# Performance work log

Hardware: AMD Instinct MI355X
Metric: run time of the kernel (lower is better)

The kernel has to match this reference:

```python
import jax, jax.numpy as jnp
import numpy as np

HEAD_SIZE = 64


def setup_inputs() -> dict:
    key = jax.random.key(0)
    k1, k2, k3, k4 = jax.random.split(key, 4)
    B, T, C, H = 8, 2048, 1024, HEAD_SIZE
    return {
        "idx": jax.random.normal(k1, (B, T, C), dtype=jnp.float32),
        "Wk": jax.random.normal(k2, (C, H), dtype=jnp.float32) * (C ** -0.5),
        "Wq": jax.random.normal(k3, (C, H), dtype=jnp.float32) * (C ** -0.5),
        "Wv": jax.random.normal(k4, (C, H), dtype=jnp.float32) * (C ** -0.5),
    }


def reference(idx, Wk, Wq, Wv):
    # idx: [B, T, C]; Wk/Wq/Wv: [C, H]
    B, T, C = idx.shape
    H = Wk.shape[1]
    k = idx @ Wk  # [B, T, H]
    q = idx @ Wq  # [B, T, H]
    v = idx @ Wv  # [B, T, H]
    # Faithful to source: wei = k @ q^T (note: k first, as written in the torch code)
    wei = jnp.einsum("bth,bsh->bts", k, q) * (H ** -0.5)  # [B, T, T]
    causal = jnp.tril(jnp.ones((T, T), dtype=bool))
    wei = jnp.where(causal, wei, -jnp.inf)
    wei = jax.nn.softmax(wei, axis=-1)
    # Dropout(0.5) treated as eval-mode identity (deterministic reference)
    out = jnp.einsum("bts,bsh->bth", wei, v)  # [B, T, H]
    return out
```

## Files before the change

kernel.cpp:

```cpp
#include <hip/hip_runtime.h>

#define B_ 8
#define T_ 2048
#define C_ 1024
#define H_ 64
#define BT_ (B_ * T_)

typedef float f32x4 __attribute__((ext_vector_type(4)));
typedef unsigned short u16x4 __attribute__((ext_vector_type(4)));
typedef unsigned short u16x8 __attribute__((ext_vector_type(8)));
typedef __bf16 bf16x8 __attribute__((ext_vector_type(8)));

static __device__ __forceinline__ unsigned short f2bf(float f) {
    unsigned int u = __builtin_bit_cast(unsigned int, f);
    u = (u + 0x7FFFu + ((u >> 16) & 1u)) >> 16;
    return (unsigned short)u;
}

static __device__ __forceinline__ f32x4 mfma16(u16x8 a, u16x8 b, f32x4 c) {
    return __builtin_amdgcn_mfma_f32_16x16x32_bf16(
        __builtin_bit_cast(bf16x8, a), __builtin_bit_cast(bf16x8, b), c, 0, 0, 0);
}

static __device__ __forceinline__ void cvtpk4(float a0, float a1, float a2, float a3,
                                              unsigned& d0, unsigned& d1) {
    asm("v_cvt_pk_bf16_f32 %0, %1, %2" : "=v"(d0) : "v"(a0), "v"(a1));
    asm("v_cvt_pk_bf16_f32 %0, %1, %2" : "=v"(d1) : "v"(a2), "v"(a3));
}

static __device__ __forceinline__ int Pof(int j) {
    return 5 - (j >= 2 ? 1 : 0) - (j >= 6 ? 1 : 0);
}
static __device__ __forceinline__ int offsof(int j) {
    return (j < 2) ? 5 * j : (j < 6 ? 4 * j + 2 : 3 * j + 8);
}

__global__ __launch_bounds__(256) void wprep(const float* __restrict__ Wk,
                                             const float* __restrict__ Wq,
                                             const float* __restrict__ Wv,
                                             unsigned short* __restrict__ wt) {
    __shared__ float tile[64][65];
    const int arr = blockIdx.x >> 4, ct = blockIdx.x & 15;
    const float* W = (arr == 0) ? Wk : ((arr == 1) ? Wq : Wv);
    const int tid = threadIdx.x;
    {
        int c = tid >> 2, seg = (tid & 3) << 4;
        const float* src = W + (size_t)(ct * 64 + c) * 64 + seg;
#pragma unroll
        for (int j = 0; j < 16; j += 4) {
            f32x4 v4 = *(const f32x4*)(src + j);
            tile[c][seg + j + 0] = v4[0];
            tile[c][seg + j + 1] = v4[1];
            tile[c][seg + j + 2] = v4[2];
            tile[c][seg + j + 3] = v4[3];
        }
    }
    __syncthreads();
    {
        int h = tid >> 2, cs = (tid & 3) << 4;
        unsigned short* dst = wt + (size_t)(arr * 64 + h) * 1024 + ct * 64 + cs;
#pragma unroll
        for (int j = 0; j < 16; ++j) dst[j] = f2bf(tile[cs + j][h]);
    }
}

__global__ __launch_bounds__(512, 4) void proj_gemm(const float* __restrict__ idx,
                                                    const unsigned short* __restrict__ wt,
                                                    unsigned short* __restrict__ kw,
                                                    unsigned short* __restrict__ qw,
                                                    unsigned short* __restrict__ vtw) {
    __shared__ unsigned short As[2][32 * 64];
    __shared__ unsigned short Bs[2][192 * 64];
    const int tid = threadIdx.x;
    const int lane = tid & 63, w = tid >> 6;
    const int g = lane >> 4, l15 = lane & 15;
    const int m0 = blockIdx.x * 32;
    const int arow = tid >> 4, aseg = tid & 15;

    f32x4 acc[3] = {};
    f32x4 areg[2];
    u16x8 breg[2][3];

    auto sload = [&](int set, int k0) {
        areg[set] = *(const f32x4*)(idx + (size_t)(m0 + arow) * 1024 + k0 + aseg * 4);
#pragma unroll
        for (int i = 0; i < 3; ++i) {
            int slot = i * 512 + tid, n = slot >> 3, u = slot & 7;
            breg[set][i] = *(const u16x8*)(wt + (size_t)n * 1024 + k0 + u * 8);
        }
    };
    auto swrite = [&](int set, int buf) {
        unsigned d0, d1;
        cvtpk4(areg[set][0], areg[set][1], areg[set][2], areg[set][3], d0, d1);
        int au = aseg >> 1, ah = aseg & 1;
        uint2 pk; pk.x = d0; pk.y = d1;
        *(uint2*)&As[buf][arow * 64 + ((au ^ (arow & 7)) * 8) + ah * 4] = pk;
#pragma unroll
        for (int i = 0; i < 3; ++i) {
            int slot = i * 512 + tid, n = slot >> 3, u = slot & 7;
            *(u16x8*)&Bs[buf][n * 64 + ((u ^ (n & 7)) * 8)] = breg[set][i];
        }
    };

    sload(0, 0);
    sload(1, 64);
    swrite(0, 0);
    __syncthreads();

    for (int kt = 0; kt < 16; ++kt) {
        const int cur = kt & 1;
        if (kt < 14) sload(cur, (kt + 2) * 64);
#pragma unroll
        for (int ks = 0; ks < 2; ++ks) {
            u16x8 a = *(const u16x8*)&As[cur][((w & 1) * 16 + l15) * 64 +
                                              (((ks * 4 + g) ^ (l15 & 7)) * 8)];
#pragma unroll
            for (int nf = 0; nf < 3; ++nf) {
                int n = (w >> 1) * 48 + nf * 16 + l15;
                u16x8 b = *(const u16x8*)&Bs[cur][n * 64 + (((ks * 4 + g) ^ (n & 7)) * 8)];
                acc[nf] = mfma16(a, b, acc[nf]);
            }
        }
        if (kt < 15) swrite(cur ^ 1, cur ^ 1);
        __syncthreads();
    }

#pragma unroll
    for (int nf = 0; nf < 3; ++nf) {
        int nb = (w >> 1) * 3 + nf;
        int arr = nb >> 2;
        int nloc = ((nb & 3) << 4) + l15;
        f32x4 ac = acc[nf];
        int row = m0 + (w & 1) * 16 + g * 4;
        if (arr == 2) {
            u16x4 pk = {f2bf(ac[0]), f2bf(ac[1]), f2bf(ac[2]), f2bf(ac[3])};
            *(u16x4*)&vtw[(size_t)nloc * BT_ + row] = pk;
        } else {
            unsigned short* dst = arr ? qw : kw;
            dst[(size_t)(row + 0) * 64 + nloc] = f2bf(ac[0]);
            dst[(size_t)(row + 1) * 64 + nloc] = f2bf(ac[1]);
            dst[(size_t)(row + 2) * 64 + nloc] = f2bf(ac[2]);
            dst[(size_t)(row + 3) * 64 + nloc] = f2bf(ac[3]);
        }
    }
}

__global__ __launch_bounds__(512, 2) void attn_part(const unsigned short* __restrict__ kw,
                                                    const unsigned short* __restrict__ qw,
                                                    const unsigned short* __restrict__ vtw,
                                                    float* __restrict__ Opart,
                                                    float* __restrict__ lpart) {
    __shared__ unsigned short q_s[2][64 * 64];
    __shared__ unsigned short v_s[2][64 * 64];
    __shared__ unsigned short p_s[8 * 32 * 64];
    const int tid = threadIdx.x;
    const int w = tid >> 6, lane = tid & 63;
    const int g = lane >> 4, l15 = lane & 15;
    const int bid = blockIdx.x;
    const int b = bid & 7;
    const int rem = bid >> 3;
    const int j = (rem < 10) ? (rem / 5) : (rem < 26 ? (rem - 2) >> 2 : (rem - 8) / 3);
    const int P = Pof(j);
    const int part = rem - offsof(j);
    const size_t base = (size_t)b * T_;
    const int tA0 = 128 * j + 16 * w;
    const int tB0 = 128 * (15 - j) + 16 * w;
    const int nS = 2 * (16 - j);
    unsigned short* p_my = p_s + w * 2048;
    const float SCL = 0.125f * 1.44269504f;
    const float MOFF = 16.0f;
    const int sr = tid >> 3, su = tid & 7;

    u16x8 kf[2][2];
#pragma unroll
    for (int tf = 0; tf < 2; ++tf) {
        const unsigned short* kr = kw + (size_t)(base + (tf ? tB0 : tA0) + l15) * 64;
        kf[tf][0] = *(const u16x8*)(kr + g * 8);
        kf[tf][1] = *(const u16x8*)(kr + 32 + g * 8);
    }

    f32x4 o[4][2] = {};
    float l_lane[2] = {0.f, 0.f};

    u16x8 tq, tv;
    auto sload = [&](int st) {
        int s0 = st << 6;
        tq = *(const u16x8*)(qw + (size_t)(base + s0 + sr) * 64 + su * 8);
        tv = *(const u16x8*)(vtw + (size_t)sr * BT_ + base + s0 + su * 8);
    };
    auto swrite = [&](int buf) {
        *(u16x8*)&q_s[buf][sr * 64 + ((su ^ (sr & 7)) * 8)] = tq;
        *(u16x8*)&v_s[buf][sr * 64 + ((su ^ (sr & 7)) * 8)] = tv;
    };

    sload(part);
    swrite(0);
    __syncthreads();

    int i = 0;
    for (int st = part; st < nS; st += P, ++i) {
        const int s0 = st << 6;
        const int buf = i & 1;
        const bool more = (st + P < nS);
        if (more) sload(st + P);
        const bool dA = (s0 <= tA0 + 15);
        const bool dB = (s0 <= tB0 + 15);

        u16x8 a[2][4];
#pragma unroll
        for (int ks = 0; ks < 2; ++ks)
#pragma unroll
            for (int sf = 0; sf < 4; ++sf)
                a[ks][sf] = *(const u16x8*)&q_s[buf][(sf * 16 + l15) * 64 +
                                                     (((ks * 4 + g) ^ (l15 & 7)) * 8)];

        f32x4 s_[4][2] = {};
        __builtin_amdgcn_s_setprio(1);
        if (dB) {
#pragma unroll
            for (int ks = 0; ks < 2; ++ks)
#pragma unroll
                for (int sf = 0; sf < 4; ++sf)
                    s_[sf][1] = mfma16(a[ks][sf], kf[1][ks], s_[sf][1]);
        }
        if (dA) {
#pragma unroll
            for (int ks = 0; ks < 2; ++ks)
#pragma unroll
                for (int sf = 0; sf < 4; ++sf)
                    s_[sf][0] = mfma16(a[ks][sf], kf[0][ks], s_[sf][0]);
        }
        __builtin_amdgcn_s_setprio(0);

#pragma unroll
        for (int tf_ = 1; tf_ >= 0; --tf_) {
            if (tf_ ? !dB : !dA) continue;
            const int tbase_ = tf_ ? tB0 : tA0;
            float pv[4][4];
#pragma unroll
            for (int sf = 0; sf < 4; ++sf)
#pragma unroll
                for (int r = 0; r < 4; ++r)
                    pv[sf][r] = exp2f(fmaf(s_[sf][tf_][r], SCL, -MOFF));
            if (s0 + 63 > tbase_) {
                const int t_ = tbase_ + l15;
#pragma unroll
                for (int sf = 0; sf < 4; ++sf)
#pragma unroll
                    for (int r = 0; r < 4; ++r) {
                        int sg = s0 + sf * 16 + g * 4 + r;
                        if (sg > t_) pv[sf][r] = 0.f;
                    }
            }
            float lacc = 0.f;
#pragma unroll
            for (int sf = 0; sf < 4; ++sf)
                lacc += (pv[sf][0] + pv[sf][1]) + (pv[sf][2] + pv[sf][3]);
            l_lane[tf_] += lacc;
            const int trow = tf_ * 16 + l15;
#pragma unroll
            for (int sf = 0; sf < 4; ++sf) {
                unsigned r0, r1;
                cvtpk4(pv[sf][0], pv[sf][1], pv[sf][2], pv[sf][3], r0, r1);
                int u16i = (sf * 2 + (g >> 1)) ^ (l15 & 7);
                uint2 pk; pk.x = r0; pk.y = r1;
                *(uint2*)&p_my[trow * 64 + u16i * 8 + (g & 1) * 4] = pk;
            }
        }

        u16x8 vf[2][4];
#pragma unroll
        for (int ks = 0; ks < 2; ++ks)
#pragma unroll
            for (int mf = 0; mf < 4; ++mf)
                vf[ks][mf] = *(const u16x8*)&v_s[buf][(mf * 16 + l15) * 64 +
                                                      (((ks * 4 + g) ^ (l15 & 7)) * 8)];
        __builtin_amdgcn_s_setprio(1);
#pragma unroll
        for (int ks = 0; ks < 2; ++ks) {
            if (dB) {
                u16x8 bp1 = *(const u16x8*)&p_my[(16 + l15) * 64 +
                                                 (((ks * 4 + g) ^ (l15 & 7)) * 8)];
#pragma unroll
                for (int mf = 0; mf < 4; ++mf)
                    o[mf][1] = mfma16(vf[ks][mf], bp1, o[mf][1]);
            }
            if (dA) {
                u16x8 bp0 = *(const u16x8*)&p_my[l15 * 64 +
                                                 (((ks * 4 + g) ^ (l15 & 7)) * 8)];
#pragma unroll
                for (int mf = 0; mf < 4; ++mf)
                    o[mf][0] = mfma16(vf[ks][mf], bp0, o[mf][0]);
            }
        }
        __builtin_amdgcn_s_setprio(0);

        if (more) swrite(buf ^ 1);
        __syncthreads();
    }

#pragma unroll
    for (int tf = 0; tf < 2; ++tf) {
        float ls = l_lane[tf];
        ls += __shfl_xor(ls, 16);
        ls += __shfl_xor(ls, 32);
        int rl = tf * 128 + w * 16 + l15;
        if (g == 0) lpart[(size_t)bid * 256 + rl] = ls;
#pragma unroll
        for (int mf = 0; mf < 4; ++mf)
            *(f32x4*)&Opart[(size_t)bid * 16384 + (size_t)rl * 64 + mf * 16 + g * 4] = o[mf][tf];
    }
}

__global__ __launch_bounds__(256) void attn_comb(const float* __restrict__ Opart,
                                                 const float* __restrict__ lpart,
                                                 float* __restrict__ out) {
    int gt = blockIdx.x * 256 + threadIdx.x;
    int row = gt >> 4;
    int h0 = (gt & 15) << 2;
    int b = row >> 11, t = row & 2047;
    int ti = t >> 7, rit = t & 127;
    int j = (ti < 8) ? ti : (15 - ti);
    int tf = (ti < 8) ? 0 : 1;
    int rl = tf * 128 + rit;
    int P = Pof(j), offs = offsof(j);
    f32x4 acc = {};
    float L = 0.f;
    for (int p = 0; p < P; ++p) {
        int pb = b + 8 * (offs + p);
        acc += *(const f32x4*)&Opart[(size_t)pb * 16384 + (size_t)rl * 64 + h0];
        L += lpart[(size_t)pb * 256 + rl];
    }
    float inv = 1.f / L;
    *(f32x4*)&out[(size_t)row * 64 + h0] = acc * inv;
}

extern "C" void kernel_launch(void* const* d_in, const int* in_sizes, int n_in,
                              void* d_out, int out_size, void* d_ws, size_t ws_size,
                              hipStream_t stream) {
    const float* idx = (const float*)d_in[0];
    const float* Wk = (const float*)d_in[1];
    const float* Wq = (const float*)d_in[2];
    const float* Wv = (const float*)d_in[3];
    float* out = (float*)d_out;

    unsigned short* wt = (unsigned short*)d_ws;
    unsigned short* kw = wt + 192 * 1024;
    unsigned short* qw = kw + (size_t)BT_ * 64;
    unsigned short* vtw = qw + (size_t)BT_ * 64;
    float* Opart = (float*)((char*)d_ws + (8u << 20));
    float* lpart = Opart + (size_t)256 * 16384;

    wprep<<<48, 256, 0, stream>>>(Wk, Wq, Wv, wt);
    proj_gemm<<<512, 512, 0, stream>>>(idx, wt, kw, qw, vtw);
    attn_part<<<256, 512, 0, stream>>>(kw, qw, vtw, Opart, lpart);
    attn_comb<<<1024, 256, 0, stream>>>(Opart, lpart, out);
}
```

Measured before the change: 50.72 us.

## Enlarge projection GEMM M-tile to 128 rows per block to reuse weight tile

The projection GEMM block now computes 128 rows instead of 32, with each wave holding a 4x3 grid of MFMA accumulators. Each staged weight tile in shared memory is therefore reused across four times more rows, cutting redundant weight loads from global memory. The cost is only 128 blocks on a GPU with many CUs, which lowers parallelism, plus more registers and LDS per block. The occupancy hint drops from 4 to 2 to match.

```diff
diff --git a/kernel.cpp b/kernel.cpp
--- a/kernel.cpp
+++ b/kernel.cpp
@@ -64,25 +64,29 @@
     }
 }
 
-__global__ __launch_bounds__(512, 4) void proj_gemm(const float* __restrict__ idx,
+__global__ __launch_bounds__(512, 2) void proj_gemm(const float* __restrict__ idx,
                                                     const unsigned short* __restrict__ wt,
                                                     unsigned short* __restrict__ kw,
                                                     unsigned short* __restrict__ qw,
                                                     unsigned short* __restrict__ vtw) {
-    __shared__ unsigned short As[2][32 * 64];
+    __shared__ unsigned short As[2][128 * 64];
     __shared__ unsigned short Bs[2][192 * 64];
     const int tid = threadIdx.x;
     const int lane = tid & 63, w = tid >> 6;
     const int g = lane >> 4, l15 = lane & 15;
-    const int m0 = blockIdx.x * 32;
-    const int arow = tid >> 4, aseg = tid & 15;
-
-    f32x4 acc[3] = {};
-    f32x4 areg[2];
+    const int m0 = blockIdx.x * 128;
+    const int arow = tid >> 2, aseg = tid & 3;
+
+    f32x4 acc[4][3] = {};
+    f32x4 areg[2][4];
     u16x8 breg[2][3];
 
     auto sload = [&](int set, int k0) {
-        areg[set] = *(const f32x4*)(idx + (size_t)(m0 + arow) * 1024 + k0 + aseg * 4);
+        const f32x4* src = (const f32x4*)(idx + (size_t)(m0 + arow) * 1024 + k0 + aseg * 16);
+        areg[set][0] = src[0];
+        areg[set][1] = src[1];
+        areg[set][2] = src[2];
+        areg[set][3] = src[3];
 #pragma unroll
         for (int i = 0; i < 3; ++i) {
             int slot = i * 512 + tid, n = slot >> 3, u = slot & 7;
@@ -90,11 +94,14 @@
         }
     };
     auto swrite = [&](int set, int buf) {
-        unsigned d0, d1;
-        cvtpk4(areg[set][0], areg[set][1], areg[set][2], areg[set][3], d0, d1);
-        int au = aseg >> 1, ah = aseg & 1;
-        uint2 pk; pk.x = d0; pk.y = d1;
-        *(uint2*)&As[buf][arow * 64 + ((au ^ (arow & 7)) * 8) + ah * 4] = pk;
+        u16x8 c0, c1;
+#pragma unroll
+        for (int e = 0; e < 4; ++e) {
+            c0[e] = f2bf(areg[set][0][e]); c0[e + 4] = f2bf(areg[set][1][e]);
+            c1[e] = f2bf(areg[set][2][e]); c1[e + 4] = f2bf(areg[set][3][e]);
+        }
+        *(u16x8*)&As[buf][arow * 64 + (((aseg * 2) ^ (arow & 7)) * 8)] = c0;
+        *(u16x8*)&As[buf][arow * 64 + (((aseg * 2 + 1) ^ (arow & 7)) * 8)] = c1;
 #pragma unroll
         for (int i = 0; i < 3; ++i) {
             int slot = i * 512 + tid, n = slot >> 3, u = slot & 7;
@@ -112,14 +119,21 @@
         if (kt < 14) sload(cur, (kt + 2) * 64);
 #pragma unroll
         for (int ks = 0; ks < 2; ++ks) {
-            u16x8 a = *(const u16x8*)&As[cur][((w & 1) * 16 + l15) * 64 +
-                                              (((ks * 4 + g) ^ (l15 & 7)) * 8)];
+            u16x8 a[4], b[3];
+#pragma unroll
+            for (int mf = 0; mf < 4; ++mf)
+                a[mf] = *(const u16x8*)&As[cur][((w & 1) * 64 + mf * 16 + l15) * 64 +
+                                                (((ks * 4 + g) ^ (l15 & 7)) * 8)];
 #pragma unroll
             for (int nf = 0; nf < 3; ++nf) {
                 int n = (w >> 1) * 48 + nf * 16 + l15;
-                u16x8 b = *(const u16x8*)&Bs[cur][n * 64 + (((ks * 4 + g) ^ (n & 7)) * 8)];
-                acc[nf] = mfma16(a, b, acc[nf]);
-            }
+                b[nf] = *(const u16x8*)&Bs[cur][n * 64 + (((ks * 4 + g) ^ (l15 & 7)) * 8)];
+            }
+#pragma unroll
+            for (int mf = 0; mf < 4; ++mf)
+#pragma unroll
+                for (int nf = 0; nf < 3; ++nf)
+                    acc[mf][nf] = mfma16(a[mf], b[nf], acc[mf][nf]);
         }
         if (kt < 15) swrite(cur ^ 1, cur ^ 1);
         __syncthreads();
@@ -130,17 +144,20 @@
         int nb = (w >> 1) * 3 + nf;
         int arr = nb >> 2;
         int nloc = ((nb & 3) << 4) + l15;
-        f32x4 ac = acc[nf];
-        int row = m0 + (w & 1) * 16 + g * 4;
-        if (arr == 2) {
-            u16x4 pk = {f2bf(ac[0]), f2bf(ac[1]), f2bf(ac[2]), f2bf(ac[3])};
-            *(u16x4*)&vtw[(size_t)nloc * BT_ + row] = pk;
-        } else {
-            unsigned short* dst = arr ? qw : kw;
-            dst[(size_t)(row + 0) * 64 + nloc] = f2bf(ac[0]);
-            dst[(size_t)(row + 1) * 64 + nloc] = f2bf(ac[1]);
-            dst[(size_t)(row + 2) * 64 + nloc] = f2bf(ac[2]);
-            dst[(size_t)(row + 3) * 64 + nloc] = f2bf(ac[3]);
+#pragma unroll
+        for (int mf = 0; mf < 4; ++mf) {
+            f32x4 ac = acc[mf][nf];
+            int row = m0 + (w & 1) * 64 + mf * 16 + g * 4;
+            if (arr == 2) {
+                u16x4 pk = {f2bf(ac[0]), f2bf(ac[1]), f2bf(ac[2]), f2bf(ac[3])};
+                *(u16x4*)&vtw[(size_t)nloc * BT_ + row] = pk;
+            } else {
+                unsigned short* dst = arr ? qw : kw;
+                dst[(size_t)(row + 0) * 64 + nloc] = f2bf(ac[0]);
+                dst[(size_t)(row + 1) * 64 + nloc] = f2bf(ac[1]);
+                dst[(size_t)(row + 2) * 64 + nloc] = f2bf(ac[2]);
+                dst[(size_t)(row + 3) * 64 + nloc] = f2bf(ac[3]);
+            }
         }
     }
 }
@@ -352,7 +369,7 @@
     float* lpart = Opart + (size_t)256 * 16384;
 
     wprep<<<48, 256, 0, stream>>>(Wk, Wq, Wv, wt);
-    proj_gemm<<<512, 512, 0, stream>>>(idx, wt, kw, qw, vtw);
+    proj_gemm<<<128, 512, 0, stream>>>(idx, wt, kw, qw, vtw);
     attn_part<<<256, 512, 0, stream>>>(kw, qw, vtw, Opart, lpart);
     attn_comb<<<1024, 256, 0, stream>>>(Opart, lpart, out);
 }
```

Result: slower. 55.68 us (+9.8%).

## Stage W, Q and V tiles via direct global-to-LDS loads

Applied to the files above, without the earlier changes.

Replaces register-staged global loads plus LDS stores with direct global-to-LDS loads (global_load_lds, 16 bytes) for the bf16 weight tiles in the projection GEMM and the Q/V tiles in the attention kernel. The XOR swizzle moves onto the global address side, so the LDS layout the consumers read stays the same. The aim is to cut VGPR pressure and the explicit ds_write instructions. The price is relying on the barrier and the compiler's vmcnt waits to order the asynchronous LDS writes correctly against the double-buffered reads.

```diff
diff --git a/kernel.cpp b/kernel.cpp
--- a/kernel.cpp
+++ b/kernel.cpp
@@ -26,6 +26,14 @@
                                               unsigned& d0, unsigned& d1) {
     asm("v_cvt_pk_bf16_f32 %0, %1, %2" : "=v"(d0) : "v"(a0), "v"(a1));
     asm("v_cvt_pk_bf16_f32 %0, %1, %2" : "=v"(d1) : "v"(a2), "v"(a3));
+}
+
+static __device__ __forceinline__ void gload_lds16(const void* g, void* l) {
+    auto gp = (const __attribute__((address_space(1))) char*)(
+        reinterpret_cast<uintptr_t>(g));
+    auto lp = (__attribute__((address_space(3))) char*)(
+        reinterpret_cast<uintptr_t>(l));
+    __builtin_amdgcn_global_load_lds(gp, lp, 16, 0, 0);
 }
 
 static __device__ __forceinline__ int Pof(int j) {
@@ -79,37 +87,38 @@
 
     f32x4 acc[3] = {};
     f32x4 areg[2];
-    u16x8 breg[2][3];
-
-    auto sload = [&](int set, int k0) {
+
+    auto sloadA = [&](int set, int k0) {
         areg[set] = *(const f32x4*)(idx + (size_t)(m0 + arow) * 1024 + k0 + aseg * 4);
-#pragma unroll
-        for (int i = 0; i < 3; ++i) {
-            int slot = i * 512 + tid, n = slot >> 3, u = slot & 7;
-            breg[set][i] = *(const u16x8*)(wt + (size_t)n * 1024 + k0 + u * 8);
-        }
     };
-    auto swrite = [&](int set, int buf) {
+    auto swriteA = [&](int set, int buf) {
         unsigned d0, d1;
         cvtpk4(areg[set][0], areg[set][1], areg[set][2], areg[set][3], d0, d1);
         int au = aseg >> 1, ah = aseg & 1;
         uint2 pk; pk.x = d0; pk.y = d1;
         *(uint2*)&As[buf][arow * 64 + ((au ^ (arow & 7)) * 8) + ah * 4] = pk;
+    };
+    auto stageB = [&](int k0, int buf) {
 #pragma unroll
         for (int i = 0; i < 3; ++i) {
-            int slot = i * 512 + tid, n = slot >> 3, u = slot & 7;
-            *(u16x8*)&Bs[buf][n * 64 + ((u ^ (n & 7)) * 8)] = breg[set][i];
+            int slot0 = i * 512 + w * 64;
+            int n = i * 64 + w * 8 + (lane >> 3);
+            int us = (lane & 7) ^ (lane >> 3);
+            gload_lds16(wt + (size_t)n * 1024 + k0 + us * 8,
+                        &Bs[buf][slot0 * 8]);
         }
     };
 
-    sload(0, 0);
-    sload(1, 64);
-    swrite(0, 0);
+    stageB(0, 0);
+    sloadA(0, 0);
+    sloadA(1, 64);
+    swriteA(0, 0);
     __syncthreads();
 
     for (int kt = 0; kt < 16; ++kt) {
         const int cur = kt & 1;
-        if (kt < 14) sload(cur, (kt + 2) * 64);
+        if (kt < 15) stageB((kt + 1) * 64, cur ^ 1);
+        if (kt < 14) sloadA(cur, (kt + 2) * 64);
 #pragma unroll
         for (int ks = 0; ks < 2; ++ks) {
             u16x8 a = *(const u16x8*)&As[cur][((w & 1) * 16 + l15) * 64 +
@@ -121,7 +130,7 @@
                 acc[nf] = mfma16(a, b, acc[nf]);
             }
         }
-        if (kt < 15) swrite(cur ^ 1, cur ^ 1);
+        if (kt < 15) swriteA(cur ^ 1, cur ^ 1);
         __syncthreads();
     }
 
@@ -169,7 +178,6 @@
     unsigned short* p_my = p_s + w * 2048;
     const float SCL = 0.125f * 1.44269504f;
     const float MOFF = 16.0f;
-    const int sr = tid >> 3, su = tid & 7;
 
     u16x8 kf[2][2];
 #pragma unroll
@@ -182,19 +190,17 @@
     f32x4 o[4][2] = {};
     float l_lane[2] = {0.f, 0.f};
 
-    u16x8 tq, tv;
-    auto sload = [&](int st) {
+    auto stageQV = [&](int st, int buf) {
         int s0 = st << 6;
-        tq = *(const u16x8*)(qw + (size_t)(base + s0 + sr) * 64 + su * 8);
-        tv = *(const u16x8*)(vtw + (size_t)sr * BT_ + base + s0 + su * 8);
+        int r = w * 8 + (lane >> 3);
+        int us = (lane & 7) ^ (lane >> 3);
+        gload_lds16(qw + (size_t)(base + s0 + r) * 64 + us * 8,
+                    &q_s[buf][w * 512]);
+        gload_lds16(vtw + (size_t)r * BT_ + base + s0 + us * 8,
+                    &v_s[buf][w * 512]);
     };
-    auto swrite = [&](int buf) {
-        *(u16x8*)&q_s[buf][sr * 64 + ((su ^ (sr & 7)) * 8)] = tq;
-        *(u16x8*)&v_s[buf][sr * 64 + ((su ^ (sr & 7)) * 8)] = tv;
-    };
-
-    sload(part);
-    swrite(0);
+
+    stageQV(part, 0);
     __syncthreads();
 
     int i = 0;
@@ -202,7 +208,7 @@
         const int s0 = st << 6;
         const int buf = i & 1;
         const bool more = (st + P < nS);
-        if (more) sload(st + P);
+        if (more) stageQV(st + P, buf ^ 1);
         const bool dA = (s0 <= tA0 + 15);
         const bool dB = (s0 <= tB0 + 15);
 
@@ -295,7 +301,6 @@
         }
         __builtin_amdgcn_s_setprio(0);
 
-        if (more) swrite(buf ^ 1);
         __syncthreads();
     }
 
```

Measured after the change: 48.90 us. -3.6%, faster.
